# Kernel optimization log

Measured on AMD Instinct MI355X. Metric: run time of the kernel, lower is better.

The kernel has to match this reference:

```python
import jax, jax.numpy as jnp
import numpy as np

D_MODEL = 1024
H = 16
DH = 64
EPS = 1e-5


def _layernorm(x, g, b):
    mu = jnp.mean(x, axis=-1, keepdims=True)
    var = jnp.var(x, axis=-1, keepdims=True)
    return (x - mu) * jax.lax.rsqrt(var + EPS) * g + b


def setup_inputs() -> dict:
    key = jax.random.key(0)
    ks = jax.random.split(key, 16)
    B, L = 4, 4096
    s = 0.02
    inp = {
        "x": jax.random.normal(ks[0], (B, L, D_MODEL), jnp.float32),
        "ln1_g": jnp.ones((D_MODEL,), jnp.float32),
        "ln1_b": jnp.zeros((D_MODEL,), jnp.float32),
        "Wq": jax.random.normal(ks[1], (D_MODEL, H * DH), jnp.float32) * s,
        "bq": jnp.zeros((H * DH,), jnp.float32),
        "Wk": jax.random.normal(ks[2], (D_MODEL, H * DH), jnp.float32) * s,
        "bk": jnp.zeros((H * DH,), jnp.float32),
        "Wv": jax.random.normal(ks[3], (D_MODEL, H * DH), jnp.float32) * s,
        "bv": jnp.zeros((H * DH,), jnp.float32),
        "Wg": jax.random.normal(ks[4], (D_MODEL, H * DH), jnp.float32) * s,
        "bg": jnp.zeros((H * DH,), jnp.float32),
        "decay_logit": jnp.zeros((H,), jnp.float32),
        "Wo": jax.random.normal(ks[5], (H * DH, D_MODEL), jnp.float32) * s,
        "bo": jnp.zeros((D_MODEL,), jnp.float32),
        "ln2_g": jnp.ones((D_MODEL,), jnp.float32),
        "ln2_b": jnp.zeros((D_MODEL,), jnp.float32),
        "W1": jax.random.normal(ks[6], (D_MODEL, 4 * D_MODEL), jnp.float32) * s,
        "b1": jnp.zeros((4 * D_MODEL,), jnp.float32),
        "W2": jax.random.normal(ks[7], (4 * D_MODEL, D_MODEL), jnp.float32) * s,
        "b2": jnp.zeros((D_MODEL,), jnp.float32),
    }
    return inp


def reference(x, ln1_g, ln1_b, Wq, bq, Wk, bk, Wv, bv, Wg, bg, decay_logit,
              Wo, bo, ln2_g, ln2_b, W1, b1, W2, b2):
    B, L, _ = x.shape
    y = _layernorm(x, ln1_g, ln1_b)
    # projections -> [L, B, H, DH] (time-major for scan)
    def proj(W, b):
        return (y @ W + b).reshape(B, L, H, DH).transpose(1, 0, 2, 3)
    q = proj(Wq, bq)
    k = proj(Wk, bk)
    v = proj(Wv, bv)
    g = jax.nn.sigmoid(y @ Wg + bg).reshape(B, L, H, DH).transpose(1, 0, 2, 3)
    decay = jax.nn.sigmoid(decay_logit)[None, :, None]  # [1,H,1]
    scale = DH ** -0.5

    def step(state, qkvg):
        q_t, k_t, v_t, g_t = qkvg
        state = decay * state + k_t * v_t          # [B,H,DH]
        out_t = g_t * q_t * state * scale
        return state, out_t

    state0 = jnp.zeros((B, H, DH), x.dtype)
    _, outs = jax.lax.scan(step, state0, (q, k, v, g))  # [L,B,H,DH]
    o = outs.transpose(1, 0, 2, 3).reshape(B, L, H * DH) @ Wo + bo
    x2 = x + o  # dropout is identity (eval / p=0)
    h = _layernorm(x2, ln2_g, ln2_b)
    ff = jax.nn.gelu(h @ W1 + b1, approximate=False) @ W2 + b2
    return x2 + ff
```

## Files before the change

kernel.cpp:

```cpp
#include <hip/hip_runtime.h>
#include <math.h>


#define D_MODEL 1024
#define LSEQ    4096
#define BATCH   4
#define NROWS   (BATCH * LSEQ)
#define HEADS   16
#define DH      64
#define CHUNK   128
#define NCH     (LSEQ / CHUNK)

typedef short  short8  __attribute__((ext_vector_type(8)));
typedef short  short4v __attribute__((ext_vector_type(4)));
typedef float  float4v __attribute__((ext_vector_type(4)));

__device__ inline short f2bf(float f) {
    unsigned u = __float_as_uint(f);
    u += 0x7fffu + ((u >> 16) & 1u);
    return (short)(u >> 16);
}
__device__ inline float bf2f(short s) {
    return __uint_as_float(((unsigned)(unsigned short)s) << 16);
}

__device__ inline void load_lds16(const short* g, short* l) {
    __builtin_amdgcn_global_load_lds(
        (const __attribute__((address_space(1))) void*)g,
        (__attribute__((address_space(3))) void*)l,
        16, 0, 0);
}

__global__ __launch_bounds__(1024) void transpose_f32_bf16(
    const float* __restrict__ in, short* __restrict__ out, int R, int C)
{
    __shared__ float tile[32][33];
    int tx = threadIdx.x, ty = threadIdx.y;
    int r = blockIdx.y * 32 + ty;
    int c = blockIdx.x * 32 + tx;
    tile[ty][tx] = in[(size_t)r * C + c];
    __syncthreads();
    out[(size_t)(blockIdx.x * 32 + ty) * R + blockIdx.y * 32 + tx] =
        f2bf(tile[tx][ty]);
}

__global__ __launch_bounds__(256) void concat_bias(
    const float* __restrict__ bq, const float* __restrict__ bk,
    const float* __restrict__ bv, const float* __restrict__ bg,
    float* __restrict__ out)
{
    int i = blockIdx.x * 256 + threadIdx.x;
    const float* src = (i < 1024) ? bq : (i < 2048) ? bk : (i < 3072) ? bv : bg;
    out[i] = src[i & 1023];
}

__global__ __launch_bounds__(256) void ln_kernel(
    const float* __restrict__ x, const float* __restrict__ g,
    const float* __restrict__ b, short* __restrict__ y)
{
    int row = blockIdx.x;
    int tid = threadIdx.x;
    const float4* xr = (const float4*)(x + (size_t)row * D_MODEL);
    float4 v = xr[tid];
    float s  = v.x + v.y + v.z + v.w;
    float ss = v.x * v.x + v.y * v.y + v.z * v.z + v.w * v.w;
    #pragma unroll
    for (int off = 32; off > 0; off >>= 1) {
        s  += __shfl_down(s, off);
        ss += __shfl_down(ss, off);
    }
    __shared__ float sbuf[8];
    int wv = tid >> 6, ln = tid & 63;
    if (ln == 0) { sbuf[wv] = s; sbuf[4 + wv] = ss; }
    __syncthreads();
    float tot  = sbuf[0] + sbuf[1] + sbuf[2] + sbuf[3];
    float tot2 = sbuf[4] + sbuf[5] + sbuf[6] + sbuf[7];
    float mu  = tot * (1.0f / D_MODEL);
    float var = tot2 * (1.0f / D_MODEL) - mu * mu;
    float rs  = rsqrtf(var + 1e-5f);
    float4 gg = ((const float4*)g)[tid];
    float4 bb = ((const float4*)b)[tid];
    short4v o;
    o.x = f2bf((v.x - mu) * rs * gg.x + bb.x);
    o.y = f2bf((v.y - mu) * rs * gg.y + bb.y);
    o.z = f2bf((v.z - mu) * rs * gg.z + bb.z);
    o.w = f2bf((v.w - mu) * rs * gg.w + bb.w);
    ((short4v*)y)[(size_t)row * 256 + tid] = o;
}

__global__ __launch_bounds__(256) void gemm_bf16(
    const short* __restrict__ A, const short* __restrict__ BT,
    const float* __restrict__ bias, const float* __restrict__ res,
    float* __restrict__ outf, short* __restrict__ outb,
    int M, int N, int K, int mode)
{
    __shared__ short As[2 * 4096];
    __shared__ short Bs[2 * 4096];

    const int gx = gridDim.x, gy = gridDim.y;
    const int lin = blockIdx.x + blockIdx.y * gx;
    const int win = 8 * gy;
    const int grp = lin / win;
    const int rem = lin - grp * win;
    const int bx = grp * 8 + (rem & 7);
    const int by = rem >> 3;

    const int tid  = threadIdx.x;
    const int row0 = bx * 128;
    const int col0 = by * 128;
    const int lane = tid & 63;
    const int wave = tid >> 6;
    const int wm = (wave & 1) << 6;
    const int wn = (wave >> 1) << 6;
    const int lm = lane & 15;
    const int q  = lane >> 4;

    float4v acc[4][4];
    #pragma unroll
    for (int i = 0; i < 4; i++)
        #pragma unroll
        for (int j = 0; j < 4; j++)
            acc[i][j] = (float4v)(0.0f);

    const int s0 = wave * 64 + lane;
    const int s1 = 256 + wave * 64 + lane;
    const int r0 = s0 >> 2, q0 = (s0 & 3) ^ ((r0 >> 1) & 3);
    const int r1 = s1 >> 2, q1 = (s1 & 3) ^ ((r1 >> 1) & 3);
    const short* gA0 = A  + (size_t)(row0 + r0) * K + q0 * 8;
    const short* gA1 = A  + (size_t)(row0 + r1) * K + q1 * 8;
    const short* gB0 = BT + (size_t)(col0 + r0) * K + q0 * 8;
    const short* gB1 = BT + (size_t)(col0 + r1) * K + q1 * 8;
    short* lA0 = As + s0 * 8;
    short* lA1 = As + s1 * 8;
    short* lB0 = Bs + s0 * 8;
    short* lB1 = Bs + s1 * 8;

    const int swz = (lm >> 1) & 3;
    const int qs  = q ^ swz;

    load_lds16(gA0, lA0);
    load_lds16(gA1, lA1);
    load_lds16(gB0, lB0);
    load_lds16(gB1, lB1);

    int p = 0;
    for (int k0 = 0; k0 < K; k0 += 32) {
        __syncthreads();
        const int kn = k0 + 32;
        const int po = p ^ 1;
        if (kn < K) {
            load_lds16(gA0 + kn, lA0 + po * 4096);
            load_lds16(gA1 + kn, lA1 + po * 4096);
            load_lds16(gB0 + kn, lB0 + po * 4096);
            load_lds16(gB1 + kn, lB1 + po * 4096);
        }
        const short* Ab = As + p * 4096;
        const short* Bb = Bs + p * 4096;

        short8 af[4], bfr[4];
        #pragma unroll
        for (int i = 0; i < 4; i++)
            af[i] = *(const short8*)&Ab[((wm + i * 16 + lm) * 4 + qs) * 8];
        #pragma unroll
        for (int j = 0; j < 4; j++)
            bfr[j] = *(const short8*)&Bb[((wn + j * 16 + lm) * 4 + qs) * 8];
        #pragma unroll
        for (int i = 0; i < 4; i++)
            #pragma unroll
            for (int j = 0; j < 4; j++)
                acc[i][j] = __builtin_amdgcn_mfma_f32_16x16x32_bf16(
                    af[i], bfr[j], acc[i][j], 0, 0, 0);
        p ^= 1;
    }

    const int r4 = (lane >> 4) << 2;
    #pragma unroll
    for (int i = 0; i < 4; i++) {
        #pragma unroll
        for (int j = 0; j < 4; j++) {
            int colg = col0 + wn + j * 16 + lm;
            float bcol = bias[colg];
            #pragma unroll
            for (int r = 0; r < 4; r++) {
                int rowg = row0 + wm + i * 16 + r4 + r;
                size_t idx = (size_t)rowg * N + colg;
                float v = acc[i][j][r] + bcol;
                if (mode == 0) {
                    if (colg >= 3072) v = 1.0f / (1.0f + expf(-v));
                    outb[idx] = f2bf(v);
                } else if (mode == 1) {
                    outf[idx] = v + res[idx];
                } else {
                    v = 0.5f * v * (1.0f + erff(v * 0.70710678118654752f));
                    outb[idx] = f2bf(v);
                }
            }
        }
    }
}

__global__ __launch_bounds__(256) void scan_pass1(
    const short* __restrict__ qkvg, const float* __restrict__ dlogit,
    float* __restrict__ carry)
{
    int j  = blockIdx.x >> 4;
    int c  = ((blockIdx.x & 15) << 8) + threadIdx.x;
    int b  = c >> 10;
    int col = c & 1023;
    float decay = 1.0f / (1.0f + expf(-dlogit[col >> 6]));
    size_t base = ((size_t)b * LSEQ + j * CHUNK) * 4096 + col;
    float s = 0.0f;
    for (int t = 0; t < CHUNK; ++t) {
        float kk = bf2f(qkvg[base + 1024]);
        float vv = bf2f(qkvg[base + 2048]);
        s = decay * s + kk * vv;
        base += 4096;
    }
    carry[j * 4096 + c] = s;
}

__global__ __launch_bounds__(256) void scan_combine(
    const float* __restrict__ carry, const float* __restrict__ dlogit,
    float* __restrict__ sinit)
{
    int c = blockIdx.x * 256 + threadIdx.x;
    float decay = 1.0f / (1.0f + expf(-dlogit[(c & 1023) >> 6]));
    float dp = powf(decay, (float)CHUNK);
    float s = 0.0f;
    for (int j = 0; j < NCH; ++j) {
        sinit[j * 4096 + c] = s;
        s = dp * s + carry[j * 4096 + c];
    }
}

__global__ __launch_bounds__(256) void scan_pass2(
    const short* __restrict__ qkvg, const float* __restrict__ dlogit,
    const float* __restrict__ sinit, short* __restrict__ att)
{
    int j  = blockIdx.x >> 4;
    int c  = ((blockIdx.x & 15) << 8) + threadIdx.x;
    int b  = c >> 10;
    int col = c & 1023;
    float decay = 1.0f / (1.0f + expf(-dlogit[col >> 6]));
    float s = sinit[j * 4096 + c];
    size_t base  = ((size_t)b * LSEQ + j * CHUNK) * 4096 + col;
    size_t obase = ((size_t)b * LSEQ + j * CHUNK) * 1024 + col;
    for (int t = 0; t < CHUNK; ++t) {
        float qq = bf2f(qkvg[base]);
        float kk = bf2f(qkvg[base + 1024]);
        float vv = bf2f(qkvg[base + 2048]);
        float gg = bf2f(qkvg[base + 3072]);
        s = decay * s + kk * vv;
        att[obase] = f2bf(gg * qq * s * 0.125f);
        base += 4096; obase += 1024;
    }
}

extern "C" void kernel_launch(void* const* d_in, const int* in_sizes, int n_in,
                              void* d_out, int out_size, void* d_ws, size_t ws_size,
                              hipStream_t stream)
{
    const float* x      = (const float*)d_in[0];
    const float* ln1_g  = (const float*)d_in[1];
    const float* ln1_b  = (const float*)d_in[2];
    const float* Wq     = (const float*)d_in[3];
    const float* bq     = (const float*)d_in[4];
    const float* Wk     = (const float*)d_in[5];
    const float* bk     = (const float*)d_in[6];
    const float* Wv     = (const float*)d_in[7];
    const float* bv     = (const float*)d_in[8];
    const float* Wg     = (const float*)d_in[9];
    const float* bg     = (const float*)d_in[10];
    const float* dlog   = (const float*)d_in[11];
    const float* Wo     = (const float*)d_in[12];
    const float* bo     = (const float*)d_in[13];
    const float* ln2_g  = (const float*)d_in[14];
    const float* ln2_b  = (const float*)d_in[15];
    const float* W1     = (const float*)d_in[16];
    const float* b1     = (const float*)d_in[17];
    const float* W2     = (const float*)d_in[18];
    const float* b2     = (const float*)d_in[19];
    float* out = (float*)d_out;

    char* ws = (char*)d_ws;
    size_t off = 0;
    auto alloc = [&](size_t bytes) -> void* {
        void* p = ws + off;
        off += (bytes + 255) & ~(size_t)255;
        return p;
    };
    short* WqkvgT = (short*)alloc((size_t)4096 * 1024 * 2);
    short* WoT    = (short*)alloc((size_t)1024 * 1024 * 2);
    short* W1T    = (short*)alloc((size_t)4096 * 1024 * 2);
    short* W2T    = (short*)alloc((size_t)1024 * 4096 * 2);
    float* biasq  = (float*)alloc((size_t)4096 * 4);
    float* carry  = (float*)alloc((size_t)NCH * 4096 * 4);
    float* sinit  = (float*)alloc((size_t)NCH * 4096 * 4);
    short* bufA   = (short*)alloc((size_t)NROWS * 1024 * 2);
    short* bufB   = (short*)alloc((size_t)NROWS * 4096 * 2);
    float* x2 = out;
    short* ybuf = bufA;
    short* att  = bufA;
    short* hbuf = bufA;
    short* qkvg = bufB;
    short* ff1  = bufB;
    (void)in_sizes; (void)n_in; (void)out_size;

    if (off > ws_size) return;

    dim3 tb(32, 32);
    transpose_f32_bf16<<<dim3(32, 32), tb, 0, stream>>>(Wq, WqkvgT + 0 * 1024 * 1024, 1024, 1024);
    transpose_f32_bf16<<<dim3(32, 32), tb, 0, stream>>>(Wk, WqkvgT + 1 * 1024 * 1024, 1024, 1024);
    transpose_f32_bf16<<<dim3(32, 32), tb, 0, stream>>>(Wv, WqkvgT + 2 * 1024 * 1024, 1024, 1024);
    transpose_f32_bf16<<<dim3(32, 32), tb, 0, stream>>>(Wg, WqkvgT + 3 * 1024 * 1024, 1024, 1024);
    transpose_f32_bf16<<<dim3(32, 32), tb, 0, stream>>>(Wo, WoT, 1024, 1024);
    transpose_f32_bf16<<<dim3(128, 32), tb, 0, stream>>>(W1, W1T, 1024, 4096);
    transpose_f32_bf16<<<dim3(32, 128), tb, 0, stream>>>(W2, W2T, 4096, 1024);
    concat_bias<<<16, 256, 0, stream>>>(bq, bk, bv, bg, biasq);

    ln_kernel<<<NROWS, 256, 0, stream>>>(x, ln1_g, ln1_b, ybuf);

    gemm_bf16<<<dim3(128, 32), 256, 0, stream>>>(
        ybuf, WqkvgT, biasq, nullptr, nullptr, qkvg, NROWS, 4096, 1024, 0);

    scan_pass1 <<<NCH * 16, 256, 0, stream>>>(qkvg, dlog, carry);
    scan_combine<<<16, 256, 0, stream>>>(carry, dlog, sinit);
    scan_pass2 <<<NCH * 16, 256, 0, stream>>>(qkvg, dlog, sinit, att);

    gemm_bf16<<<dim3(128, 8), 256, 0, stream>>>(
        att, WoT, bo, x, x2, nullptr, NROWS, 1024, 1024, 1);

    ln_kernel<<<NROWS, 256, 0, stream>>>(x2, ln2_g, ln2_b, hbuf);

    gemm_bf16<<<dim3(128, 32), 256, 0, stream>>>(
        hbuf, W1T, b1, nullptr, nullptr, ff1, NROWS, 4096, 1024, 2);

    gemm_bf16<<<dim3(128, 8), 256, 0, stream>>>(
        ff1, W2T, b2, x2, out, nullptr, NROWS, 1024, 4096, 1);
}
```

Measured before the change: 1.051 ms.

## Triple-buffer GEMM LDS tiles with vmcnt-based waits and remap block swizzle

```diff
diff --git a/kernel.cpp b/kernel.cpp
--- a/kernel.cpp
+++ b/kernel.cpp
@@ -94,16 +94,21 @@
     float* __restrict__ outf, short* __restrict__ outb,
     int M, int N, int K, int mode)
 {
-    __shared__ short As[2 * 4096];
-    __shared__ short Bs[2 * 4096];
-
-    const int gx = gridDim.x, gy = gridDim.y;
-    const int lin = blockIdx.x + blockIdx.y * gx;
-    const int win = 8 * gy;
-    const int grp = lin / win;
-    const int rem = lin - grp * win;
-    const int bx = grp * 8 + (rem & 7);
-    const int by = rem >> 3;
+    __shared__ short As[3 * 4096];
+    __shared__ short Bs[3 * 4096];
+
+    {
+    }
+    const int MBX = gridDim.x, NBY = gridDim.y;
+    const int lin = blockIdx.x + blockIdx.y * MBX;
+    const int winsz = 8 * NBY;
+    const int w = lin / winsz;
+    const int r = lin - w * winsz;
+    const int xcd = r & 7;
+    const int t   = r >> 3;
+    const int ys  = (NBY >= 8) ? (NBY >> 3) : 1;
+    const int by  = xcd * ys + (t & (ys - 1));
+    const int bx  = w * 8 + (t / ys);
 
     const int tid  = threadIdx.x;
     const int row0 = bx * 128;
@@ -142,20 +147,25 @@
     load_lds16(gA1, lA1);
     load_lds16(gB0, lB0);
     load_lds16(gB1, lB1);
-
-    int p = 0;
+    load_lds16(gA0 + 32, lA0 + 4096);
+    load_lds16(gA1 + 32, lA1 + 4096);
+    load_lds16(gB0 + 32, lB0 + 4096);
+    load_lds16(gB1 + 32, lB1 + 4096);
+
+    int cur = 0;
     for (int k0 = 0; k0 < K; k0 += 32) {
-        __syncthreads();
-        const int kn = k0 + 32;
-        const int po = p ^ 1;
-        if (kn < K) {
-            load_lds16(gA0 + kn, lA0 + po * 4096);
-            load_lds16(gA1 + kn, lA1 + po * 4096);
-            load_lds16(gB0 + kn, lB0 + po * 4096);
-            load_lds16(gB1 + kn, lB1 + po * 4096);
-        }
-        const short* Ab = As + p * 4096;
-        const short* Bb = Bs + p * 4096;
+        asm volatile("s_waitcnt vmcnt(4)\n\ts_barrier" ::: "memory");
+
+        int kn = k0 + 64; if (kn >= K) kn -= K;
+        int nx = cur + 2; if (nx >= 3) nx -= 3;
+        const int nb = nx * 4096;
+        load_lds16(gA0 + kn, lA0 + nb);
+        load_lds16(gA1 + kn, lA1 + nb);
+        load_lds16(gB0 + kn, lB0 + nb);
+        load_lds16(gB1 + kn, lB1 + nb);
+
+        const short* Ab = As + cur * 4096;
+        const short* Bb = Bs + cur * 4096;
 
         short8 af[4], bfr[4];
         #pragma unroll
@@ -170,8 +180,10 @@
             for (int j = 0; j < 4; j++)
                 acc[i][j] = __builtin_amdgcn_mfma_f32_16x16x32_bf16(
                     af[i], bfr[j], acc[i][j], 0, 0, 0);
-        p ^= 1;
-    }
+
+        cur = (cur + 1 == 3) ? 0 : cur + 1;
+    }
+    asm volatile("s_waitcnt vmcnt(0)" ::: "memory");
 
     const int r4 = (lane >> 4) << 2;
     #pragma unroll
@@ -181,10 +193,10 @@
             int colg = col0 + wn + j * 16 + lm;
             float bcol = bias[colg];
             #pragma unroll
-            for (int r = 0; r < 4; r++) {
-                int rowg = row0 + wm + i * 16 + r4 + r;
+            for (int r2 = 0; r2 < 4; r2++) {
+                int rowg = row0 + wm + i * 16 + r4 + r2;
                 size_t idx = (size_t)rowg * N + colg;
-                float v = acc[i][j][r] + bcol;
+                float v = acc[i][j][r2] + bcol;
                 if (mode == 0) {
                     if (colg >= 3072) v = 1.0f / (1.0f + expf(-v));
                     outb[idx] = f2bf(v);
```

New measurement: 1.145 ms. +9.0%, slower.
